# Kernel optimization log

Hardware: AMD Instinct MI355X
Metric: run time of the kernel (lower is better)

Reference implementation:

```python
import jax, jax.numpy as jnp
import numpy as np

Z, Y, X = 16, 128, 128
B = 2
N_R, N_L = 12000, 20000   # active voxels per batch element (radar / lidar)
C = 64
IN_DIM = 4
NUM_LAYER = 2
K_LIST = (64, 32)         # knn fan-out = 64 / 2**layer
EPS = 1e-5


def _make_voxels(rng, n_per_batch):
    # unique voxel coords per batch, sorted by linear index (batch-major rows)
    out = []
    for b in range(B):
        lin = np.sort(rng.choice(Z * Y * X, size=n_per_batch, replace=False))
        z = lin // (Y * X); y = (lin // X) % Y; x = lin % X
        out.append(np.stack([np.full(n_per_batch, b), z, y, x], 1))
    return np.concatenate(out, 0).astype(np.int32)


def _nbr_map(coords):
    # 3x3x3 submanifold-conv rulebook: row index of each neighbor, -1 if absent
    b = coords[:, 0].astype(np.int64); z = coords[:, 1]; y = coords[:, 2]; x = coords[:, 3]
    keys = ((b * Z + z) * Y + y) * X + x  # globally sorted
    N = coords.shape[0]
    nbr = np.full((N, 27), -1, np.int64)
    k = 0
    for dz in (-1, 0, 1):
        for dy in (-1, 0, 1):
            for dx in (-1, 0, 1):
                nz, ny, nx = z + dz, y + dy, x + dx
                ok = (nz >= 0) & (nz < Z) & (ny >= 0) & (ny < Y) & (nx >= 0) & (nx < X)
                cand = ((b * Z + nz) * Y + ny) * X + nx
                pos = np.searchsorted(keys, cand)
                pos_c = np.clip(pos, 0, N - 1)
                hit = ok & (keys[pos_c] == cand)
                nbr[:, k] = np.where(hit, pos_c, -1)
                k += 1
    return nbr


def setup_inputs() -> dict:
    rng = np.random.default_rng(0)
    key = jax.random.key(0)
    ks = jax.random.split(key, 16)
    coordsR = _make_voxels(rng, N_R)
    coordsL = _make_voxels(rng, N_L)
    nbrR = _nbr_map(coordsR)
    nbrL = _nbr_map(coordsL)
    NLt = B * N_L
    # knn indices (global row ids into radar rows of same batch)
    knn0 = coordsL[:, 0:1].astype(np.int64) * N_R + rng.integers(0, N_R, (NLt, K_LIST[0]))
    knn1 = coordsL[:, 0:1].astype(np.int64) * N_R + rng.integers(0, N_R, (NLt, K_LIST[1]))
    sc = 1.0 / np.sqrt(27 * C).astype(np.float32)
    inp = {
        "featR": jax.random.normal(ks[0], (B * N_R, IN_DIM), jnp.float32),
        "featL": jax.random.normal(ks[1], (NLt, IN_DIM), jnp.float32),
        "img": jax.random.normal(ks[2], (B, 512), jnp.float32),
        "Win": jax.random.normal(ks[3], (2, IN_DIM, C), jnp.float32) * 0.1,
        "bin_": jnp.zeros((2, C), jnp.float32),
        # [layer, branch(R/L), conv(sp,subm_a,subm_b), 27, Cin, Cout]
        "Wconv": jax.random.normal(ks[4], (NUM_LAYER, 2, 3, 27, C, C), jnp.float32) * sc,
        "bconv": jnp.zeros((NUM_LAYER, 2, 3, C), jnp.float32),
        "bng": jnp.ones((NUM_LAYER, 2, 3, C), jnp.float32),
        "bnb": jnp.zeros((NUM_LAYER, 2, 3, C), jnp.float32),
        "Wimg": jax.random.normal(ks[5], (NUM_LAYER, 512, C), jnp.float32) * 0.05,
        "bimg": jnp.zeros((NUM_LAYER, C), jnp.float32),
        "Wval": jax.random.normal(ks[6], (NUM_LAYER, C, C), jnp.float32) * 0.125,
        "bval": jnp.zeros((NUM_LAYER, C), jnp.float32),
        "Wgate": jax.random.normal(ks[7], (NUM_LAYER, 2 * C, C), jnp.float32) * 0.09,
        "bgate": jnp.zeros((NUM_LAYER, C), jnp.float32),
        "Wbev": jax.random.normal(ks[8], (NUM_LAYER, 2, C * Z, C, 3, 3), jnp.float32) * (1.0 / np.sqrt(C * Z * 9).astype(np.float32)),
        "bbev": jnp.zeros((NUM_LAYER, 2, C), jnp.float32),
        "bntg": jnp.ones((NUM_LAYER, 2, C), jnp.float32),
        "bntb": jnp.zeros((NUM_LAYER, 2, C), jnp.float32),
        "nbrR": jnp.asarray(nbrR),
        "nbrL": jnp.asarray(nbrL),
        "knn0": jnp.asarray(knn0),
        "knn1": jnp.asarray(knn1),
        "coordsR": jnp.asarray(coordsR),
        "coordsL": jnp.asarray(coordsL),
    }
    return inp


def _bn1d(f, g, b):
    m = f.mean(0)
    v = f.var(0)
    return (f - m) / jnp.sqrt(v + EPS) * g + b


def _sconv(f, nbr, W, bias):
    # gather-scatter sparse 3D conv: out[n] = sum_k W[k] @ f[nbr[n,k]]
    mask = (nbr >= 0)[..., None].astype(f.dtype)
    g = f[jnp.clip(nbr, 0)] * mask                 # [N, 27, C]
    return jnp.einsum('nkc,kcd->nd', g, W) + bias


def _branch_block(f, nbr, Wc, bc, g, bt):
    # spconv -> bn -> relu, subm_a -> bn -> relu, subm_b -> bn -> relu
    for j in range(3):
        f = jax.nn.relu(_bn1d(_sconv(f, nbr, Wc[j], bc[j]), g[j], bt[j]))
    return f


def _to_bev(f, coords, Wt, bt, gg, gb):
    dense = jnp.zeros((B, Z, Y, X, C), f.dtype).at[
        coords[:, 0], coords[:, 1], coords[:, 2], coords[:, 3]].add(f)
    x2 = dense.transpose(0, 4, 1, 2, 3).reshape(B, C * Z, Y, X)  # 'b c z y x -> b (c z) y x'
    # ConvTranspose2d(k=3, s=1, p=1) == conv with swapped-IO, spatially flipped kernel, pad 1
    Wk = jnp.transpose(Wt, (1, 0, 2, 3))[:, :, ::-1, ::-1]
    out = jax.lax.conv_general_dilated(x2, Wk, (1, 1), ((1, 1), (1, 1)),
                                       dimension_numbers=('NCHW', 'OIHW', 'NCHW'))
    out = out + bt[:, None, None]
    m = out.mean((0, 2, 3), keepdims=True)
    v = out.var((0, 2, 3), keepdims=True)
    out = (out - m) / jnp.sqrt(v + EPS) * gg[:, None, None] + gb[:, None, None]
    return jax.nn.relu(out)


def reference(featR, featL, img, Win, bin_, Wconv, bconv, bng, bnb, Wimg, bimg,
              Wval, bval, Wgate, bgate, Wbev, bbev, bntg, bntb,
              nbrR, nbrL, knn0, knn1, coordsR, coordsL):
    fR = featR @ Win[0] + bin_[0]   # input_convR (1x1x1)
    fL = featL @ Win[1] + bin_[1]   # input_convL (1x1x1)
    knns = (knn0, knn1)
    bidL = coordsL[:, 0]
    bevs = []
    for l in range(NUM_LAYER):
        fR = _branch_block(fR, nbrR, Wconv[l, 0], bconv[l, 0], bng[l, 0], bnb[l, 0])
        fL = _branch_block(fL, nbrL, Wconv[l, 1], bconv[l, 1], bng[l, 1], bnb[l, 1])
        # knn cross-attention fusion: lidar queries K nearest radar voxels
        key = fR[knns[l]]                                        # [NL, K, C]
        val = jnp.einsum('nkc,cd->nkd', key, Wval[l]) + bval[l]
        attn = jax.nn.softmax(jnp.einsum('nc,nkc->nk', fL, key), axis=-1)
        fused = jnp.einsum('nk,nkd->nd', attn, val)
        imgf = jax.nn.sigmoid(img @ Wimg[l] + bimg[l])           # [B, C] weather condition
        fused = fused * imgf[bidL]
        gate = jax.nn.sigmoid(jnp.concatenate([fL, fused], -1) @ Wgate[l] + bgate[l])
        fL = fL + gate * fused
        bevs.append(_to_bev(fR, coordsR, Wbev[l, 0], bbev[l, 0], bntg[l, 0], bntb[l, 0]))
        bevs.append(_to_bev(fL, coordsL, Wbev[l, 1], bbev[l, 1], bntg[l, 1], bntb[l, 1]))
    return jnp.concatenate(bevs, axis=1)  # [B, 4*C, Y, X]
```

## Files before the change

### kernel.cpp

```cpp
#include <hip/hip_runtime.h>
#include <math.h>

#define NRT 24000
#define NLT 40000

static __device__ __forceinline__ float sigmoidf_(float x){ return 1.0f/(1.0f+expf(-x)); }

static __device__ __forceinline__ int xcd_swz(int bid, int nwg){
  int q = nwg>>3, r = nwg&7, x = bid&7, i = bid>>3;
  return (x<r ? x*(q+1) : r*(q+1)+(x-r)*q) + i;
}

__global__ void k_proj(const float* __restrict__ feat, const float* __restrict__ W,
                       const float* __restrict__ bias, float* __restrict__ out, int N){
  int i = blockIdx.x*256 + threadIdx.x;
  if (i >= N*64) return;
  int n = i >> 6, c = i & 63;
  const float* f = feat + n*4;
  out[i] = fmaf(f[0], W[c], fmaf(f[1], W[64+c], fmaf(f[2], W[128+c], fmaf(f[3], W[192+c], bias[c]))));
}

__global__ void k_kmask(const int* __restrict__ nbr, int NG, int* __restrict__ kmask){
  int g = blockIdx.x*64 + threadIdx.x;
  if (g >= NG) return;
  int m = 0;
  for (int v=0;v<4;v++){
    const int* row = nbr + (size_t)(g*4+v)*27;
    for (int k=0;k<27;k++) if (row[k] >= 0) m |= (1<<k);
  }
  kmask[g] = m;
}

__global__ void k_sconv(const float* __restrict__ fin, const int* __restrict__ nbr,
                        const int* __restrict__ kmask, const float* __restrict__ W,
                        float* __restrict__ fout, int N){
  int d = threadIdx.x & 63;
  int blk = xcd_swz(blockIdx.x, gridDim.x);
  int g = blk*4 + (threadIdx.x>>6);
  int n0 = g*4;
  float acc[4] = {0.f,0.f,0.f,0.f};
  int m = kmask[g];
  while (m){
    int k = __builtin_ctz(m); m &= m-1;
    const float* w = W + k*4096 + d;
    float wr[64];
    #pragma unroll
    for (int c=0;c<64;c++) wr[c] = w[c*64];
    #pragma unroll
    for (int v=0;v<4;v++){
      int nb = nbr[(size_t)(n0+v)*27 + k];
      if (nb >= 0){
        const float* fr = fin + (size_t)nb*64;
        #pragma unroll
        for (int c=0;c<64;c+=4){
          float4 fv = *reinterpret_cast<const float4*>(fr + c);
          acc[v] = fmaf(fv.x, wr[c+0], acc[v]);
          acc[v] = fmaf(fv.y, wr[c+1], acc[v]);
          acc[v] = fmaf(fv.z, wr[c+2], acc[v]);
          acc[v] = fmaf(fv.w, wr[c+3], acc[v]);
        }
      }
    }
  }
  #pragma unroll
  for (int v=0;v<4;v++) fout[(size_t)(n0+v)*64 + d] = acc[v];
}

__global__ void k_colsum(const float* __restrict__ f, int N, float* __restrict__ partial){
  int d = threadIdx.x & 63, sub = threadIdx.x >> 6;
  float s=0.f, s2=0.f;
  for (int n = blockIdx.x*4 + sub; n < N; n += 1024){
    float v = f[(size_t)n*64+d];
    s += v; s2 = fmaf(v,v,s2);
  }
  __shared__ float ls[4][64], ls2[4][64];
  ls[sub][d]=s; ls2[sub][d]=s2;
  __syncthreads();
  if (sub==0){
    s  = ls[0][d]+ls[1][d]+ls[2][d]+ls[3][d];
    s2 = ls2[0][d]+ls2[1][d]+ls2[2][d]+ls2[3][d];
    partial[(blockIdx.x*64+d)*2+0]=s;
    partial[(blockIdx.x*64+d)*2+1]=s2;
  }
}

__global__ void k_bnfin(const float* __restrict__ partial, int nblk, float invN,
                        const float* __restrict__ g, const float* __restrict__ b,
                        float* __restrict__ mv){
  int d = threadIdx.x;
  float s=0.f, s2=0.f;
  for (int i=0;i<nblk;i++){ s += partial[(i*64+d)*2]; s2 += partial[(i*64+d)*2+1]; }
  float mean = s*invN;
  float var  = s2*invN - mean*mean;
  float rstd = 1.0f/sqrtf(var + 1e-5f);
  float sc = g[d]*rstd;
  mv[d*2]   = sc;
  mv[d*2+1] = b[d] - mean*sc;
}

__global__ void k_bnrelu(float* __restrict__ f, const float* __restrict__ mv, int total){
  int i = blockIdx.x*256+threadIdx.x;
  if (i>=total) return;
  int c = i & 63;
  float v = fmaf(f[i], mv[c*2], mv[c*2+1]);
  f[i] = v>0.f? v:0.f;
}

__global__ void k_imgf(const float* __restrict__ img, const float* __restrict__ Wimg,
                       const float* __restrict__ bimg, float* __restrict__ imgf){
  int t = threadIdx.x;
  int b = t>>6, c = t&63;
  float s = bimg[c];
  const float* ir = img + b*512;
  for (int j=0;j<512;j++) s = fmaf(ir[j], Wimg[j*64+c], s);
  imgf[b*64+c] = sigmoidf_(s);
}

__global__ void k_attn(float* __restrict__ fL, const float* __restrict__ fR,
                       const int* __restrict__ knn, const int* __restrict__ coordsL,
                       const float* __restrict__ Wval, const float* __restrict__ bval,
                       const float* __restrict__ Wgate, const float* __restrict__ bgate,
                       const float* __restrict__ imgf, int K){
  __shared__ float keys[64*65];
  __shared__ float fls[64];
  __shared__ float aw[64];
  __shared__ float wks[64];
  __shared__ float fus[64];
  int n = blockIdx.x, t = threadIdx.x;
  float fl = fL[(size_t)n*64+t];
  fls[t] = fl;
  const int* kn = knn + (size_t)n*K;
  for (int k=0;k<K;k++){
    int r = kn[k];
    keys[k*65+t] = fR[(size_t)r*64+t];
  }
  __syncthreads();
  float s = -1e30f;
  if (t < K){
    const float* kr = keys + t*65;
    float a0 = 0.f;
    #pragma unroll
    for (int c=0;c<64;c++) a0 = fmaf(fls[c], kr[c], a0);
    s = a0;
  }
  float mx = s;
  #pragma unroll
  for (int m=32;m;m>>=1) mx = fmaxf(mx, __shfl_xor(mx, m, 64));
  float e = (t<K) ? expf(s-mx) : 0.f;
  float se = e;
  #pragma unroll
  for (int m=32;m;m>>=1) se += __shfl_xor(se, m, 64);
  aw[t] = e/se;
  __syncthreads();
  float wk = 0.f;
  for (int k=0;k<K;k++) wk = fmaf(aw[k], keys[k*65+t], wk);
  wks[t] = wk;
  __syncthreads();
  float fu = bval[t];
  #pragma unroll
  for (int c=0;c<64;c++) fu = fmaf(wks[c], Wval[c*64+t], fu);
  int bid = coordsL[n*4];
  fu *= imgf[bid*64+t];
  fus[t] = fu;
  __syncthreads();
  float gs = bgate[t];
  #pragma unroll
  for (int c=0;c<64;c++) gs = fmaf(fls[c], Wgate[c*64+t], gs);
  #pragma unroll
  for (int c=0;c<64;c++) gs = fmaf(fus[c], Wgate[(64+c)*64+t], gs);
  float gate = sigmoidf_(gs);
  fL[(size_t)n*64+t] = fl + gate*fu;
}

__global__ void k_grid(const int* __restrict__ coords, int N, int* __restrict__ grid){
  int n = blockIdx.x*256+threadIdx.x;
  if (n>=N) return;
  int b=coords[n*4], z=coords[n*4+1], y=coords[n*4+2], x=coords[n*4+3];
  grid[((b*128+y)*128+x)*16+z] = n;
}

__global__ void k_colbuild(const int* __restrict__ grid, int* __restrict__ ccnt,
                           int* __restrict__ cent){
  int col = blockIdx.x*256+threadIdx.x;
  if (col >= 2*128*128) return;
  const int* g = grid + col*16;
  int c=0;
  for (int z=0;z<16;z++){ int v=g[z]; if (v>=0) cent[col*16 + (c++)] = (v<<4)|z; }
  ccnt[col]=c;
}

__global__ void k_wt2(const float* __restrict__ Wbev, float* __restrict__ Wt2){
  int i = blockIdx.x*256+threadIdx.x;
  if (i >= 4*9*16*64*64) return;
  int o = i & 63; int r = i >> 6;
  int c = r & 63; r >>= 6;
  int z = r & 15; r >>= 4;
  int q = r % 9; int ls = r / 9;
  int qy = q/3, qx = q%3;
  int ky = 2-qy, kx = 2-qx;
  Wt2[i] = Wbev[(size_t)ls*589824 + (size_t)(c*16+z)*576 + o*9 + ky*3 + kx];
}

__global__ void k_bev(const float* __restrict__ f, const int* __restrict__ ccnt,
                      const int* __restrict__ cent, const float* __restrict__ Wt2,
                      float* __restrict__ outp){
  int p = xcd_swz(blockIdx.x, gridDim.x);
  int b = p>>14, y = (p>>7)&127, x = p&127;
  int t = threadIdx.x;
  float acc = 0.f;
  #pragma unroll
  for (int q=0;q<9;q++){
    int y2 = y + q/3 - 1, x2 = x + q%3 - 1;
    if ((unsigned)y2 < 128u && (unsigned)x2 < 128u){
      int col = ((b<<7)+y2)*128 + x2;
      int cn = ccnt[col];
      const int* ce = cent + col*16;
      for (int i=0;i<cn;i++){
        int e = ce[i];
        int rid = e>>4, z = e&15;
        const float* fr = f + (size_t)rid*64;
        const float* w = Wt2 + (size_t)(((q<<4)+z)<<12) + t;
        #pragma unroll
        for (int c=0;c<64;c+=4){
          float4 fv = *reinterpret_cast<const float4*>(fr + c);
          acc = fmaf(fv.x, w[(c+0)<<6], acc);
          acc = fmaf(fv.y, w[(c+1)<<6], acc);
          acc = fmaf(fv.z, w[(c+2)<<6], acc);
          acc = fmaf(fv.w, w[(c+3)<<6], acc);
        }
      }
    }
  }
  outp[(size_t)b*(256*16384) + (size_t)t*16384 + (p & 16383)] = acc;
}

__global__ void k_bevstat(const float* __restrict__ outp, const float* __restrict__ g,
                          const float* __restrict__ b, float* __restrict__ mv){
  int ch = blockIdx.x, t = threadIdx.x;
  float s=0.f, s2=0.f;
  for (int bb=0;bb<2;bb++){
    const float* base = outp + (size_t)bb*(256*16384) + (size_t)ch*16384;
    for (int p=t;p<16384;p+=256){ float v = base[p]; s+=v; s2=fmaf(v,v,s2); }
  }
  __shared__ float ls[256], ls2[256];
  ls[t]=s; ls2[t]=s2; __syncthreads();
  for (int m=128;m;m>>=1){ if (t<m){ ls[t]+=ls[t+m]; ls2[t]+=ls2[t+m]; } __syncthreads(); }
  if (t==0){
    float mean = ls[0]*(1.0f/32768.0f);
    float var  = ls2[0]*(1.0f/32768.0f) - mean*mean;
    float rstd = 1.0f/sqrtf(var+1e-5f);
    float sc = g[ch]*rstd;
    mv[ch*2]=sc; mv[ch*2+1]=b[ch]-mean*sc;
  }
}

__global__ void k_bevbn(float* __restrict__ outp, const float* __restrict__ mv){
  int i = blockIdx.x*256+threadIdx.x;
  if (i >= 2*64*16384) return;
  int bb = i>>20; int r = i & ((1<<20)-1);
  int ch = r>>14; int p = r&16383;
  float* a = outp + (size_t)bb*(256*16384) + (size_t)ch*16384 + p;
  float v = fmaf(*a, mv[ch*2], mv[ch*2+1]);
  *a = v>0.f? v:0.f;
}

extern "C" void kernel_launch(void* const* d_in, const int* in_sizes, int n_in,
                              void* d_out, int out_size, void* d_ws, size_t ws_size,
                              hipStream_t stream){
  const float* featR = (const float*)d_in[0];
  const float* featL = (const float*)d_in[1];
  const float* img   = (const float*)d_in[2];
  const float* Win   = (const float*)d_in[3];
  const float* bin_  = (const float*)d_in[4];
  const float* Wconv = (const float*)d_in[5];
  const float* bng   = (const float*)d_in[7];
  const float* bnb   = (const float*)d_in[8];
  const float* Wimg  = (const float*)d_in[9];
  const float* bimg  = (const float*)d_in[10];
  const float* Wval  = (const float*)d_in[11];
  const float* bval  = (const float*)d_in[12];
  const float* Wgate = (const float*)d_in[13];
  const float* bgate = (const float*)d_in[14];
  const float* Wbev  = (const float*)d_in[15];
  const float* bntg  = (const float*)d_in[17];
  const float* bntb  = (const float*)d_in[18];
  const int* nbrR    = (const int*)d_in[19];
  const int* nbrL    = (const int*)d_in[20];
  const int* knn0    = (const int*)d_in[21];
  const int* knn1    = (const int*)d_in[22];
  const int* coordsR = (const int*)d_in[23];
  const int* coordsL = (const int*)d_in[24];
  float* outp = (float*)d_out;

  char* w = (char*)d_ws;
  auto alloc = [&](size_t bytes){ char* p = w; w += (bytes + 255) & ~(size_t)255; return p; };
  float* fRa = (float*)alloc((size_t)NRT*64*4);
  float* fRb = (float*)alloc((size_t)NRT*64*4);
  float* fLa = (float*)alloc((size_t)NLT*64*4);
  float* fLb = (float*)alloc((size_t)NLT*64*4);
  int*   gridR = (int*)alloc((size_t)2*128*128*16*4);
  int*   gridL = (int*)alloc((size_t)2*128*128*16*4);
  float* Wt2 = (float*)alloc((size_t)4*9*16*64*64*4);
  float* imgfbuf = (float*)alloc(2*64*4);
  float* partial = (float*)alloc((size_t)256*64*2*4);
  float* mv = (float*)alloc(64*2*4);
  int* kmaskR = (int*)alloc((size_t)(NRT/4)*4);
  int* kmaskL = (int*)alloc((size_t)(NLT/4)*4);
  int* ccntR = (int*)alloc((size_t)2*128*128*4);
  int* ccntL = (int*)alloc((size_t)2*128*128*4);
  int* centR = (int*)alloc((size_t)2*128*128*16*4);
  int* centL = (int*)alloc((size_t)2*128*128*16*4);

  hipMemsetAsync(gridR, 0xFF, (size_t)2*128*128*16*4, stream);
  hipMemsetAsync(gridL, 0xFF, (size_t)2*128*128*16*4, stream);
  k_grid<<<(NRT+255)/256,256,0,stream>>>(coordsR, NRT, gridR);
  k_grid<<<(NLT+255)/256,256,0,stream>>>(coordsL, NLT, gridL);
  k_colbuild<<<(2*128*128+255)/256,256,0,stream>>>(gridR, ccntR, centR);
  k_colbuild<<<(2*128*128+255)/256,256,0,stream>>>(gridL, ccntL, centL);
  k_kmask<<<((NRT/4)+63)/64,64,0,stream>>>(nbrR, NRT/4, kmaskR);
  k_kmask<<<((NLT/4)+63)/64,64,0,stream>>>(nbrL, NLT/4, kmaskL);
  k_wt2<<<(4*9*16*64*64+255)/256,256,0,stream>>>(Wbev, Wt2);

  k_proj<<<(NRT*64+255)/256,256,0,stream>>>(featR, Win,     bin_,    fRa, NRT);
  k_proj<<<(NLT*64+255)/256,256,0,stream>>>(featL, Win+256, bin_+64, fLa, NLT);

  float* fRcur=fRa; float* fRalt=fRb; float* fLcur=fLa; float* fLalt=fLb;
  for (int l=0;l<2;l++){
    for (int j=0;j<3;j++){
      const float* Wc = Wconv + (size_t)(((l*2+0)*3+j)*27)*4096;
      k_sconv<<<NRT/16,256,0,stream>>>(fRcur, nbrR, kmaskR, Wc, fRalt, NRT);
      k_colsum<<<256,256,0,stream>>>(fRalt, NRT, partial);
      k_bnfin<<<1,64,0,stream>>>(partial, 256, 1.0f/NRT,
                                 bng + ((l*2+0)*3+j)*64, bnb + ((l*2+0)*3+j)*64, mv);
      k_bnrelu<<<(NRT*64+255)/256,256,0,stream>>>(fRalt, mv, NRT*64);
      float* tmp=fRcur; fRcur=fRalt; fRalt=tmp;
    }
    for (int j=0;j<3;j++){
      const float* Wc = Wconv + (size_t)(((l*2+1)*3+j)*27)*4096;
      k_sconv<<<NLT/16,256,0,stream>>>(fLcur, nbrL, kmaskL, Wc, fLalt, NLT);
      k_colsum<<<256,256,0,stream>>>(fLalt, NLT, partial);
      k_bnfin<<<1,64,0,stream>>>(partial, 256, 1.0f/NLT,
                                 bng + ((l*2+1)*3+j)*64, bnb + ((l*2+1)*3+j)*64, mv);
      k_bnrelu<<<(NLT*64+255)/256,256,0,stream>>>(fLalt, mv, NLT*64);
      float* tmp=fLcur; fLcur=fLalt; fLalt=tmp;
    }
    k_imgf<<<1,128,0,stream>>>(img, Wimg + (size_t)l*512*64, bimg + l*64, imgfbuf);
    const int* knn = (l==0)? knn0 : knn1;
    int K = (l==0)? 64 : 32;
    k_attn<<<NLT,64,0,stream>>>(fLcur, fRcur, knn, coordsL,
                                Wval + (size_t)l*4096, bval + l*64,
                                Wgate + (size_t)l*8192, bgate + l*64,
                                imgfbuf, K);
    {
      float* op = outp + (size_t)(2*l)*64*16384;
      const float* wt = Wt2 + (size_t)(l*2+0)*9*16*4096;
      k_bev<<<2*128*128,64,0,stream>>>(fRcur, ccntR, centR, wt, op);
      k_bevstat<<<64,256,0,stream>>>(op, bntg + (l*2+0)*64, bntb + (l*2+0)*64, mv);
      k_bevbn<<<(2*64*16384+255)/256,256,0,stream>>>(op, mv);
    }
    {
      float* op = outp + (size_t)(2*l+1)*64*16384;
      const float* wt = Wt2 + (size_t)(l*2+1)*9*16*4096;
      k_bev<<<2*128*128,64,0,stream>>>(fLcur, ccntL, centL, wt, op);
      k_bevstat<<<64,256,0,stream>>>(op, bntg + (l*2+1)*64, bntb + (l*2+1)*64, mv);
      k_bevbn<<<(2*64*16384+255)/256,256,0,stream>>>(op, mv);
    }
  }
}
```

Measured before the change: 3.076 ms.

## Vectorize conv and BEV weight loads; tile BEV over four x-columns per block

Both weight tensors are re-laid out so each thread loads float4 weights holding four input channels, cutting scalar load count in the sparse conv and the BEV projection. The sparse conv no longer preloads 64 weight registers per offset. It streams float4 weights per neighbor, which may increase weight traffic but lowers register pressure. The BEV kernel now computes four adjacent x outputs per block, so each voxel's features are loaded once and reused across the overlapping 3x3 windows, and the result is written with a float4 store. The price is more register state per thread and extra preprocessing kernels for the weight transposes.

```diff
diff --git a/kernel.cpp b/kernel.cpp
--- a/kernel.cpp
+++ b/kernel.cpp
@@ -31,39 +31,53 @@
   kmask[g] = m;
 }
 
+__global__ void k_wc(const float* __restrict__ Wconv, float* __restrict__ WcT){
+  int i = blockIdx.x*256+threadIdx.x;
+  if (i >= 12*27*16*64*4) return;
+  int j = i & 3; int r = i >> 2;
+  int d = r & 63; r >>= 6;
+  int c4 = r & 15; r >>= 4;
+  int k = r % 27; int lc = r / 27;
+  WcT[i] = Wconv[(size_t)lc*110592 + (size_t)k*4096 + (size_t)(4*c4+j)*64 + d];
+}
+
 __global__ void k_sconv(const float* __restrict__ fin, const int* __restrict__ nbr,
                         const int* __restrict__ kmask, const float* __restrict__ W,
                         float* __restrict__ fout, int N){
-  int d = threadIdx.x & 63;
+  int t = threadIdx.x & 63;
   int blk = xcd_swz(blockIdx.x, gridDim.x);
   int g = blk*4 + (threadIdx.x>>6);
   int n0 = g*4;
-  float acc[4] = {0.f,0.f,0.f,0.f};
+  float4 av[4];
+  #pragma unroll
+  for (int v=0;v<4;v++) av[v] = make_float4(0.f,0.f,0.f,0.f);
+  const int* nrow = nbr + (size_t)n0*27;
   int m = kmask[g];
   while (m){
     int k = __builtin_ctz(m); m &= m-1;
-    const float* w = W + k*4096 + d;
-    float wr[64];
-    #pragma unroll
-    for (int c=0;c<64;c++) wr[c] = w[c*64];
+    const float4* w4 = reinterpret_cast<const float4*>(W + (size_t)k*4096) + t;
     #pragma unroll
     for (int v=0;v<4;v++){
-      int nb = nbr[(size_t)(n0+v)*27 + k];
+      int nb = nrow[27*v + k];
       if (nb >= 0){
-        const float* fr = fin + (size_t)nb*64;
+        const float4* fr = reinterpret_cast<const float4*>(fin + (size_t)nb*64);
+        float4 a = make_float4(0.f,0.f,0.f,0.f);
         #pragma unroll
-        for (int c=0;c<64;c+=4){
-          float4 fv = *reinterpret_cast<const float4*>(fr + c);
-          acc[v] = fmaf(fv.x, wr[c+0], acc[v]);
-          acc[v] = fmaf(fv.y, wr[c+1], acc[v]);
-          acc[v] = fmaf(fv.z, wr[c+2], acc[v]);
-          acc[v] = fmaf(fv.w, wr[c+3], acc[v]);
+        for (int c4=0;c4<16;c4++){
+          float4 w = w4[c4*64];
+          float4 f = fr[c4];
+          a.x = fmaf(f.x, w.x, a.x);
+          a.y = fmaf(f.y, w.y, a.y);
+          a.z = fmaf(f.z, w.z, a.z);
+          a.w = fmaf(f.w, w.w, a.w);
         }
+        av[v].x += a.x; av[v].y += a.y; av[v].z += a.z; av[v].w += a.w;
       }
     }
   }
   #pragma unroll
-  for (int v=0;v<4;v++) fout[(size_t)(n0+v)*64 + d] = acc[v];
+  for (int v=0;v<4;v++)
+    fout[(size_t)(n0+v)*64 + t] = (av[v].x+av[v].y)+(av[v].z+av[v].w);
 }
 
 __global__ void k_colsum(const float* __restrict__ f, int N, float* __restrict__ partial){
@@ -189,49 +203,72 @@
   ccnt[col]=c;
 }
 
-__global__ void k_wt2(const float* __restrict__ Wbev, float* __restrict__ Wt2){
+__global__ void k_wt3(const float* __restrict__ Wbev, float* __restrict__ Wt3){
   int i = blockIdx.x*256+threadIdx.x;
-  if (i >= 4*9*16*64*64) return;
-  int o = i & 63; int r = i >> 6;
-  int c = r & 63; r >>= 6;
+  if (i >= 4*9*16*16*64*4) return;
+  int j = i & 3; int r = i >> 2;
+  int o = r & 63; r >>= 6;
+  int c4 = r & 15; r >>= 4;
   int z = r & 15; r >>= 4;
   int q = r % 9; int ls = r / 9;
-  int qy = q/3, qx = q%3;
-  int ky = 2-qy, kx = 2-qx;
-  Wt2[i] = Wbev[(size_t)ls*589824 + (size_t)(c*16+z)*576 + o*9 + ky*3 + kx];
+  int c = 4*c4 + j;
+  int ky = 2-q/3, kx = 2-q%3;
+  Wt3[i] = Wbev[(size_t)ls*589824 + (size_t)(c*16+z)*576 + o*9 + ky*3 + kx];
 }
 
 __global__ void k_bev(const float* __restrict__ f, const int* __restrict__ ccnt,
-                      const int* __restrict__ cent, const float* __restrict__ Wt2,
+                      const int* __restrict__ cent, const float* __restrict__ Wt,
                       float* __restrict__ outp){
-  int p = xcd_swz(blockIdx.x, gridDim.x);
-  int b = p>>14, y = (p>>7)&127, x = p&127;
+  int blk = xcd_swz(blockIdx.x, gridDim.x);
+  int b = blk>>12; int rem = blk&4095; int y = rem>>5; int x0 = (rem&31)<<2;
   int t = threadIdx.x;
-  float acc = 0.f;
-  #pragma unroll
-  for (int q=0;q<9;q++){
-    int y2 = y + q/3 - 1, x2 = x + q%3 - 1;
-    if ((unsigned)y2 < 128u && (unsigned)x2 < 128u){
-      int col = ((b<<7)+y2)*128 + x2;
+  float4 av[4];
+  #pragma unroll
+  for (int v=0;v<4;v++) av[v] = make_float4(0.f,0.f,0.f,0.f);
+  #pragma unroll
+  for (int dy=-1;dy<=1;dy++){
+    int y2 = y+dy;
+    if ((unsigned)y2 >= 128u) continue;
+    int qb = (dy+1)*3;
+    for (int cx=x0-1; cx<=x0+4; cx++){
+      if ((unsigned)cx >= 128u) continue;
+      int col = ((b<<7)+y2)*128 + cx;
       int cn = ccnt[col];
       const int* ce = cent + col*16;
       for (int i=0;i<cn;i++){
         int e = ce[i];
         int rid = e>>4, z = e&15;
-        const float* fr = f + (size_t)rid*64;
-        const float* w = Wt2 + (size_t)(((q<<4)+z)<<12) + t;
+        const float4* fr = reinterpret_cast<const float4*>(f + (size_t)rid*64);
+        float4 fv[16];
         #pragma unroll
-        for (int c=0;c<64;c+=4){
-          float4 fv = *reinterpret_cast<const float4*>(fr + c);
-          acc = fmaf(fv.x, w[(c+0)<<6], acc);
-          acc = fmaf(fv.y, w[(c+1)<<6], acc);
-          acc = fmaf(fv.z, w[(c+2)<<6], acc);
-          acc = fmaf(fv.w, w[(c+3)<<6], acc);
+        for (int c4=0;c4<16;c4++) fv[c4] = fr[c4];
+        #pragma unroll
+        for (int v=0;v<4;v++){
+          int dx = cx - (x0+v);
+          if (dx>=-1 && dx<=1){
+            int q = qb + dx + 1;
+            const float4* w4 = reinterpret_cast<const float4*>(Wt + (size_t)(((q<<4)+z)<<12)) + t;
+            float4 a = make_float4(0.f,0.f,0.f,0.f);
+            #pragma unroll
+            for (int c4=0;c4<16;c4++){
+              float4 w = w4[c4*64];
+              a.x = fmaf(fv[c4].x, w.x, a.x);
+              a.y = fmaf(fv[c4].y, w.y, a.y);
+              a.z = fmaf(fv[c4].z, w.z, a.z);
+              a.w = fmaf(fv[c4].w, w.w, a.w);
+            }
+            av[v].x += a.x; av[v].y += a.y; av[v].z += a.z; av[v].w += a.w;
+          }
         }
       }
     }
   }
-  outp[(size_t)b*(256*16384) + (size_t)t*16384 + (p & 16383)] = acc;
+  float4 o4;
+  o4.x = (av[0].x+av[0].y)+(av[0].z+av[0].w);
+  o4.y = (av[1].x+av[1].y)+(av[1].z+av[1].w);
+  o4.z = (av[2].x+av[2].y)+(av[2].z+av[2].w);
+  o4.w = (av[3].x+av[3].y)+(av[3].z+av[3].w);
+  *reinterpret_cast<float4*>(outp + (size_t)b*(256*16384) + (size_t)t*16384 + y*128 + x0) = o4;
 }
 
 __global__ void k_bevstat(const float* __restrict__ outp, const float* __restrict__ g,
@@ -300,7 +337,8 @@
   float* fLb = (float*)alloc((size_t)NLT*64*4);
   int*   gridR = (int*)alloc((size_t)2*128*128*16*4);
   int*   gridL = (int*)alloc((size_t)2*128*128*16*4);
-  float* Wt2 = (float*)alloc((size_t)4*9*16*64*64*4);
+  float* Wt3 = (float*)alloc((size_t)4*9*16*16*64*4*4);
+  float* WcT = (float*)alloc((size_t)12*27*16*64*4*4);
   float* imgfbuf = (float*)alloc(2*64*4);
   float* partial = (float*)alloc((size_t)256*64*2*4);
   float* mv = (float*)alloc(64*2*4);
@@ -319,7 +357,8 @@
   k_colbuild<<<(2*128*128+255)/256,256,0,stream>>>(gridL, ccntL, centL);
   k_kmask<<<((NRT/4)+63)/64,64,0,stream>>>(nbrR, NRT/4, kmaskR);
   k_kmask<<<((NLT/4)+63)/64,64,0,stream>>>(nbrL, NLT/4, kmaskL);
-  k_wt2<<<(4*9*16*64*64+255)/256,256,0,stream>>>(Wbev, Wt2);
+  k_wt3<<<(4*9*16*16*64*4+255)/256,256,0,stream>>>(Wbev, Wt3);
+  k_wc<<<(12*27*16*64*4+255)/256,256,0,stream>>>(Wconv, WcT);
 
   k_proj<<<(NRT*64+255)/256,256,0,stream>>>(featR, Win,     bin_,    fRa, NRT);
   k_proj<<<(NLT*64+255)/256,256,0,stream>>>(featL, Win+256, bin_+64, fLa, NLT);
@@ -327,7 +366,7 @@
   float* fRcur=fRa; float* fRalt=fRb; float* fLcur=fLa; float* fLalt=fLb;
   for (int l=0;l<2;l++){
     for (int j=0;j<3;j++){
-      const float* Wc = Wconv + (size_t)(((l*2+0)*3+j)*27)*4096;
+      const float* Wc = WcT + (size_t)((l*2+0)*3+j)*110592;
       k_sconv<<<NRT/16,256,0,stream>>>(fRcur, nbrR, kmaskR, Wc, fRalt, NRT);
       k_colsum<<<256,256,0,stream>>>(fRalt, NRT, partial);
       k_bnfin<<<1,64,0,stream>>>(partial, 256, 1.0f/NRT,
@@ -336,7 +375,7 @@
       float* tmp=fRcur; fRcur=fRalt; fRalt=tmp;
     }
     for (int j=0;j<3;j++){
-      const float* Wc = Wconv + (size_t)(((l*2+1)*3+j)*27)*4096;
+      const float* Wc = WcT + (size_t)((l*2+1)*3+j)*110592;
       k_sconv<<<NLT/16,256,0,stream>>>(fLcur, nbrL, kmaskL, Wc, fLalt, NLT);
       k_colsum<<<256,256,0,stream>>>(fLalt, NLT, partial);
       k_bnfin<<<1,64,0,stream>>>(partial, 256, 1.0f/NLT,
@@ -353,15 +392,15 @@
                                 imgfbuf, K);
     {
       float* op = outp + (size_t)(2*l)*64*16384;
-      const float* wt = Wt2 + (size_t)(l*2+0)*9*16*4096;
-      k_bev<<<2*128*128,64,0,stream>>>(fRcur, ccntR, centR, wt, op);
+      const float* wt = Wt3 + (size_t)(l*2+0)*9*16*4096;
+      k_bev<<<2*128*32,64,0,stream>>>(fRcur, ccntR, centR, wt, op);
       k_bevstat<<<64,256,0,stream>>>(op, bntg + (l*2+0)*64, bntb + (l*2+0)*64, mv);
       k_bevbn<<<(2*64*16384+255)/256,256,0,stream>>>(op, mv);
     }
     {
       float* op = outp + (size_t)(2*l+1)*64*16384;
-      const float* wt = Wt2 + (size_t)(l*2+1)*9*16*4096;
-      k_bev<<<2*128*128,64,0,stream>>>(fLcur, ccntL, centL, wt, op);
+      const float* wt = Wt3 + (size_t)(l*2+1)*9*16*4096;
+      k_bev<<<2*128*32,64,0,stream>>>(fLcur, ccntL, centL, wt, op);
       k_bevstat<<<64,256,0,stream>>>(op, bntg + (l*2+1)*64, bntb + (l*2+1)*64, mv);
       k_bevbn<<<(2*64*16384+255)/256,256,0,stream>>>(op, mv);
     }
```

Measured after the change: 3.225 ms. +4.8%, slower.
